# Kernel optimization log

Hardware: AMD Instinct MI355X
Metric: run time of the kernel (lower is better)

Reference implementation:

```python
import jax, jax.numpy as jnp
import numpy as np

N_NODES = 100000
N_EDGES = 1600000
C = 256            # in_channels == out_channels
NUM_BUNDLES = 64
BUNDLE_DIM = 2
NUM_GRAPHS = 128
BN_EPS = 1e-5


def setup_inputs() -> dict:
    key = jax.random.key(0)
    ks = jax.random.split(key, 12)
    x = jax.random.normal(ks[0], (N_NODES, C), dtype=jnp.float32)
    edge_index = jax.random.randint(ks[1], (2, N_EDGES), 0, N_NODES, dtype=jnp.int64)
    batch = jnp.sort(jax.random.randint(ks[2], (N_NODES,), 0, NUM_GRAPHS, dtype=jnp.int64))
    s = 0.05
    # struct_enc MLP: Linear(C, 2*NB) -> GELU -> Linear(2*NB, NB)
    se_w1 = jax.random.normal(ks[3], (C, 2 * NUM_BUNDLES), dtype=jnp.float32) * s
    se_b1 = jnp.zeros((2 * NUM_BUNDLES,), dtype=jnp.float32)
    se_w2 = jax.random.normal(ks[4], (2 * NUM_BUNDLES, NUM_BUNDLES), dtype=jnp.float32) * s
    se_b2 = jnp.zeros((NUM_BUNDLES,), dtype=jnp.float32)
    # LimConv.lin: Linear(C, C)
    lin_w = jax.random.normal(ks[5], (C, C), dtype=jnp.float32) * s
    lin_b = jnp.zeros((C,), dtype=jnp.float32)
    # BatchNorm1d affine params
    bn_gamma = jnp.ones((C,), dtype=jnp.float32)
    bn_beta = jnp.zeros((C,), dtype=jnp.float32)
    return {"x": x, "edge_index": edge_index, "batch": batch,
            "se_w1": se_w1, "se_b1": se_b1, "se_w2": se_w2, "se_b2": se_b2,
            "lin_w": lin_w, "lin_b": lin_b, "bn_gamma": bn_gamma, "bn_beta": bn_beta}


def _lim_layer(x, batch, se_w1, se_b1, se_w2, se_b2, lin_w, lin_b, bn_gamma, bn_beta):
    n = x.shape[0]
    # vector field: [N, NB, 2, fiber]
    vf = x.reshape(n, NUM_BUNDLES, BUNDLE_DIM, -1)
    # struct_enc MLP -> per-bundle angle (tanh-squashed), euler map to SO(2)
    h1 = jax.nn.gelu(x @ se_w1 + se_b1, approximate=False)
    ang = jnp.tanh(h1 @ se_w2 + se_b2)          # [N, NB]
    c, s = jnp.cos(ang), jnp.sin(ang)
    # R[n,b] = [[c,-s],[s,c]]  -> [N, NB, 2, 2]
    rot = jnp.stack([jnp.stack([c, -s], axis=-1),
                     jnp.stack([s, c], axis=-1)], axis=-2)
    # rotate fibers
    vf = jnp.einsum('nbij,nbjf->nbif', rot, vf)
    h = vf.reshape(n, C) @ lin_w + lin_b
    # global mean pool over graphs, then broadcast back to nodes
    sums = jax.ops.segment_sum(h, batch, num_segments=NUM_GRAPHS)
    cnts = jax.ops.segment_sum(jnp.ones((n,), h.dtype), batch, num_segments=NUM_GRAPHS)
    hmean = sums / jnp.maximum(cnts, 1.0)[:, None]
    h = hmean[batch]
    # inverse rotation (R^T)
    vf = h.reshape(n, NUM_BUNDLES, BUNDLE_DIM, -1)
    vf = jnp.einsum('nbji,nbjf->nbif', rot, vf)
    h = vf.reshape(n, C)
    # residual (dim_in == dim_out)
    h = x + h
    # dropout p=0 / eval -> identity. BatchNorm1d with batch statistics.
    mu = jnp.mean(h, axis=0)
    var = jnp.var(h, axis=0)
    h = (h - mu) * jax.lax.rsqrt(var + BN_EPS) * bn_gamma + bn_beta
    return h


def reference(x, edge_index, batch, se_w1, se_b1, se_w2, se_b2, lin_w, lin_b, bn_gamma, bn_beta):
    # edge_index is unused when num_gnn == 0 (struct_enc is an MLP), as in the source.
    del edge_index
    return _lim_layer(x, batch, se_w1, se_b1, se_w2, se_b2, lin_w, lin_b, bn_gamma, bn_beta)
```

## Files before the change

kernel.cpp:

```cpp
#include <hip/hip_runtime.h>
#include <hip/hip_bf16.h>
#include <math.h>

#define N_NODES 100000
#define C 256
#define NB 64
#define H1D 128
#define NG 128
#define BN_EPS 1e-5f

#define BLKN 32
#define NBLK1 (N_NODES / BLKN)

#define GREC 769

#define OFF_GSUMS 0
#define OFF_BNSUM (NG * GREC)
#define OFF_BNSQ  (OFF_BNSUM + 256)
#define ZERO_FLOATS (OFF_BNSQ + 256)
#define OFF_HMEAN ZERO_FLOATS
#define OFF_WT1   (OFF_HMEAN + NG * C)
#define OFF_WT2   (OFF_WT1 + 16896)
#define OFF_CSN   (OFF_WT2 + 4352)

#define WT1_LD 264
#define WT2_LD 136
#define XS_LD  272

typedef __attribute__((ext_vector_type(8))) short bf16x8;
typedef __attribute__((ext_vector_type(4))) float f32x4;

struct __align__(8) bf4 { __hip_bfloat16 x, y, z, w; };

__device__ __forceinline__ float bf2f(__hip_bfloat16 h) { return __bfloat162float(h); }

__device__ __forceinline__ float fast_tanh(float y) {
    float e = __expf(2.f * y);
    return 1.f - 2.f / (e + 1.f);
}
__device__ __forceinline__ float fast_gelu(float v) {
    float u = 0.7978845608f * (v + 0.044715f * v * v * v);
    return 0.5f * v * (1.f + fast_tanh(u));
}

__global__ __launch_bounds__(256)
void k0_prep(const float* __restrict__ W1, const float* __restrict__ W2,
             __hip_bfloat16* __restrict__ Wt1, __hip_bfloat16* __restrict__ Wt2)
{
    const int t0 = threadIdx.x + blockIdx.x * 256;
    const int stride = gridDim.x * 256;
    for (int i = t0; i < 128 * 256; i += stride) {
        int n = i >> 8, k = i & 255;
        Wt1[n * WT1_LD + k] = __float2bfloat16(W1[k * 128 + n]);
    }
    for (int i = t0; i < 64 * 128; i += stride) {
        int n = i >> 7, k = i & 127;
        Wt2[n * WT2_LD + k] = __float2bfloat16(W2[k * 64 + n]);
    }
}

__global__ __launch_bounds__(256, 6)
void k1_angles_rot_pool(const float* __restrict__ x,
                        const int* __restrict__ batch,
                        const __hip_bfloat16* __restrict__ Wt1g,
                        const float* __restrict__ b1,
                        const __hip_bfloat16* __restrict__ Wt2g,
                        const float* __restrict__ b2,
                        float* __restrict__ gsums,
                        float* __restrict__ bnsum, float* __restrict__ bnsq,
                        __hip_bfloat16* __restrict__ csng)
{
    __shared__ __hip_bfloat16 xs[BLKN][XS_LD];
    __shared__ char sm_u[BLKN * WT2_LD * 2];
    __shared__ int gsh[BLKN];
    auto h1s = (__hip_bfloat16 (*)[WT2_LD])sm_u;
    auto csn = (__hip_bfloat16 (*)[132])sm_u;

    const int t = threadIdx.x;
    const int w = t >> 6;
    const int l = t & 63;
    const int lo = l & 15, quad = l >> 4;
    const int n0 = blockIdx.x * BLKN;

    #pragma unroll
    for (int m = 0; m < 8; ++m) {
        int idx = t + m * 256;
        int r = idx >> 6, c4 = (idx & 63) * 4;
        float4 v = *(const float4*)(x + (size_t)(n0 + r) * C + c4);
        bf4 pk;
        pk.x = __float2bfloat16(v.x); pk.y = __float2bfloat16(v.y);
        pk.z = __float2bfloat16(v.z); pk.w = __float2bfloat16(v.w);
        *(bf4*)&xs[r][c4] = pk;
    }
    if (t < BLKN) gsh[t] = batch[n0 + t];
    __syncthreads();

    const short* w1base = (const short*)Wt1g + (w * 32 + lo) * WT1_LD + quad * 8;
    f32x4 acc1[2][2];
    #pragma unroll
    for (int mt = 0; mt < 2; ++mt) { acc1[mt][0] = (f32x4)0.f; acc1[mt][1] = (f32x4)0.f; }
    #pragma unroll
    for (int k = 0; k < 8; ++k) {
        bf16x8 bA = *(const bf16x8*)(w1base + k * 32);
        bf16x8 bB = *(const bf16x8*)(w1base + 16 * WT1_LD + k * 32);
        #pragma unroll
        for (int mt = 0; mt < 2; ++mt) {
            bf16x8 afr = *(const bf16x8*)&xs[mt * 16 + lo][k * 32 + quad * 8];
            acc1[mt][0] = __builtin_amdgcn_mfma_f32_16x16x32_bf16(afr, bA, acc1[mt][0], 0, 0, 0);
            acc1[mt][1] = __builtin_amdgcn_mfma_f32_16x16x32_bf16(afr, bB, acc1[mt][1], 0, 0, 0);
        }
    }
    #pragma unroll
    for (int nt = 0; nt < 2; ++nt) {
        const float bb = b1[w * 32 + nt * 16 + lo];
        #pragma unroll
        for (int mt = 0; mt < 2; ++mt) {
            #pragma unroll
            for (int r = 0; r < 4; ++r) {
                float v = fast_gelu(acc1[mt][nt][r] + bb);
                h1s[mt * 16 + quad * 4 + r][w * 32 + nt * 16 + lo] = __float2bfloat16(v);
            }
        }
    }
    __syncthreads();

    const int mw = w >> 1;
    const int nb0 = (w & 1) * 32;
    const short* w2base = (const short*)Wt2g + (nb0 + lo) * WT2_LD + quad * 8;
    f32x4 acc2[2];
    acc2[0] = (f32x4)0.f; acc2[1] = (f32x4)0.f;
    #pragma unroll
    for (int k = 0; k < 4; ++k) {
        bf16x8 afr = *(const bf16x8*)&h1s[mw * 16 + lo][k * 32 + quad * 8];
        bf16x8 bA = *(const bf16x8*)(w2base + k * 32);
        bf16x8 bB = *(const bf16x8*)(w2base + 16 * WT2_LD + k * 32);
        acc2[0] = __builtin_amdgcn_mfma_f32_16x16x32_bf16(afr, bA, acc2[0], 0, 0, 0);
        acc2[1] = __builtin_amdgcn_mfma_f32_16x16x32_bf16(afr, bB, acc2[1], 0, 0, 0);
    }
    __syncthreads();

    #pragma unroll
    for (int nt = 0; nt < 2; ++nt) {
        const int col = nb0 + nt * 16 + lo;
        const float bb = b2[col];
        #pragma unroll
        for (int r = 0; r < 4; ++r) {
            float a = fast_tanh(acc2[nt][r] + bb);
            union { unsigned int u; __hip_bfloat16 h[2]; } p;
            p.h[0] = __float2bfloat16(__cosf(a));
            p.h[1] = __float2bfloat16(__sinf(a));
            *(unsigned int*)&csn[mw * 16 + quad * 4 + r][2 * col] = p.u;
        }
    }
    __syncthreads();

    #pragma unroll
    for (int m = 0; m < 4; ++m) {
        int idx = t + m * 256;
        int row = idx >> 5;
        int q = (idx & 31);
        uint2 v = *(const uint2*)&csn[row][q * 4];
        *(uint2*)(csng + (size_t)(n0 + row) * 128 + q * 4) = v;
    }

    {
        const int c = t;
        const int b = c >> 2;
        const int idx2 = c & 3;
        float xc_a = 0.f, xs_a = 0.f, xm = 0.f, xq = 0.f, st = 0.f, rcnt = 0.f;
        int gprev = gsh[0];
        #pragma unroll 8
        for (int r = 0; r < BLKN; ++r) {
            const int g = gsh[r];
            if (g != gprev) {
                float* rec = gsums + (size_t)gprev * GREC;
                atomicAdd(&rec[c], xc_a);
                atomicAdd(&rec[256 + c], xs_a);
                atomicAdd(&rec[512 + t], st);
                if (t == 0) atomicAdd(&rec[768], rcnt);
                xc_a = 0.f; xs_a = 0.f; st = 0.f; rcnt = 0.f; gprev = g;
            }
            const float xv = bf2f(xs[r][c]);
            union { unsigned int u; __hip_bfloat16 h[2]; } cs;
            cs.u = *(const unsigned int*)&csn[r][2 * b];
            const float cv = bf2f(cs.h[0]);
            const float sv = bf2f(cs.h[1]);
            xc_a += xv * cv;
            xs_a += xv * sv;
            xm += xv;
            xq += xv * xv;
            st += (idx2 == 0) ? cv : (idx2 == 1) ? sv : (idx2 == 2) ? cv * cv : cv * sv;
            rcnt += 1.f;
        }
        float* rec = gsums + (size_t)gprev * GREC;
        atomicAdd(&rec[c], xc_a);
        atomicAdd(&rec[256 + c], xs_a);
        atomicAdd(&rec[512 + t], st);
        if (t == 0) atomicAdd(&rec[768], rcnt);
        atomicAdd(&bnsum[c], xm);
        atomicAdd(&bnsq[c], xq);
    }
}

__global__ __launch_bounds__(256)
void k2_hmean_stats(const float* __restrict__ gsums,
                    const float* __restrict__ lin_w, const float* __restrict__ lin_b,
                    float* __restrict__ hmean,
                    float* __restrict__ bnsum, float* __restrict__ bnsq)
{
    __shared__ float xc[C], xsv[C], bs4[C], grot[C], hm[C];
    __shared__ float cnt_sh;
    const int g = blockIdx.x;
    const int t = threadIdx.x;
    const float* rec = gsums + (size_t)g * GREC;
    xc[t]  = rec[t];
    xsv[t] = rec[256 + t];
    bs4[t] = rec[512 + t];
    if (t == 0) cnt_sh = rec[768];
    __syncthreads();

    const int b = t >> 2, idx2 = t & 3, i2 = idx2 >> 1;
    grot[t] = (i2 == 0) ? (xc[t] - xsv[t + 2]) : (xsv[t - 2] + xc[t]);
    __syncthreads();

    float a0 = 0.f, a1 = 0.f, a2 = 0.f, a3 = 0.f;
    #pragma unroll 4
    for (int k = 0; k < C; k += 4) {
        a0 += grot[k + 0] * lin_w[(size_t)(k + 0) * C + t];
        a1 += grot[k + 1] * lin_w[(size_t)(k + 1) * C + t];
        a2 += grot[k + 2] * lin_w[(size_t)(k + 2) * C + t];
        a3 += grot[k + 3] * lin_w[(size_t)(k + 3) * C + t];
    }
    const float cnt = cnt_sh;
    const float hv = (cnt > 0.f) ? ((a0 + a1 + a2 + a3) / cnt + lin_b[t]) : 0.f;
    hm[t] = hv;
    hmean[g * C + t] = hv;
    __syncthreads();

    if (cnt > 0.f) {
        const int f = idx2 & 1;
        const float h0 = hm[4 * b + f];
        const float h1 = hm[4 * b + 2 + f];
        const float CV = bs4[4 * b + 0], SV = bs4[4 * b + 1];
        const float CC = bs4[4 * b + 2], CS = bs4[4 * b + 3];
        const float SS = cnt - CC;
        float sumc, sqc;
        if (i2 == 0) {
            sumc = h0 * CV + h1 * SV;
            sqc  = 2.f * (h0 * xc[t] + h1 * xsv[t])
                 + h0 * h0 * CC + 2.f * h0 * h1 * CS + h1 * h1 * SS;
        } else {
            sumc = -h0 * SV + h1 * CV;
            sqc  = 2.f * (-h0 * xsv[t] + h1 * xc[t])
                 + h0 * h0 * SS - 2.f * h0 * h1 * CS + h1 * h1 * CC;
        }
        atomicAdd(&bnsum[t], sumc);
        atomicAdd(&bnsq[t], sqc);
    }
}

__global__ __launch_bounds__(256, 4)
void k4_fused(const float* __restrict__ x,
              const int* __restrict__ batch,
              const __hip_bfloat16* __restrict__ csng,
              const float* __restrict__ hmean,
              const float* __restrict__ bnsum, const float* __restrict__ bnsq,
              const float* __restrict__ gamma, const float* __restrict__ beta,
              float* __restrict__ out)
{
    __shared__ float mul_s[C], add_s[C];
    const int t = threadIdx.x;
    {
        const float inv_n = 1.0f / (float)N_NODES;
        const float mu = bnsum[t] * inv_n;
        const float var = bnsq[t] * inv_n - mu * mu;
        const float inv = rsqrtf(var + BN_EPS);
        const float m = gamma[t] * inv;
        mul_s[t] = m;
        add_s[t] = beta[t] - mu * m;
    }
    __syncthreads();
    const int s = t >> 6;
    const int cg = t & 63;
    const float4 mm = *(const float4*)&mul_s[cg * 4];
    const float4 aa = *(const float4*)&add_s[cg * 4];

    for (int base = blockIdx.x * 4; base < N_NODES; base += gridDim.x * 4) {
        const int n = base + s;
        if (n < N_NODES) {
            const int g = batch[n];
            const float4 hm = *(const float4*)(hmean + (size_t)g * C + cg * 4);
            union { unsigned int u; __hip_bfloat16 h[2]; } cs;
            cs.u = *(const unsigned int*)(csng + (size_t)n * 128 + cg * 2);
            const float cv = bf2f(cs.h[0]);
            const float sv = bf2f(cs.h[1]);
            const float4 xv = *(const float4*)(x + (size_t)n * C + cg * 4);
            float4 o;
            o.x = (xv.x + cv * hm.x + sv * hm.z) * mm.x + aa.x;
            o.y = (xv.y + cv * hm.y + sv * hm.w) * mm.y + aa.y;
            o.z = (xv.z - sv * hm.x + cv * hm.z) * mm.z + aa.z;
            o.w = (xv.w - sv * hm.y + cv * hm.w) * mm.w + aa.w;
            *(float4*)(out + (size_t)n * C + cg * 4) = o;
        }
    }
}

extern "C" void kernel_launch(void* const* d_in, const int* in_sizes, int n_in,
                              void* d_out, int out_size, void* d_ws, size_t ws_size,
                              hipStream_t stream)
{
    const float* x      = (const float*)d_in[0];
    const int* batch    = (const int*)d_in[2];
    const float* W1     = (const float*)d_in[3];
    const float* b1     = (const float*)d_in[4];
    const float* W2     = (const float*)d_in[5];
    const float* b2     = (const float*)d_in[6];
    const float* lin_w  = (const float*)d_in[7];
    const float* lin_b  = (const float*)d_in[8];
    const float* gamma  = (const float*)d_in[9];
    const float* beta   = (const float*)d_in[10];

    float* ws    = (float*)d_ws;
    float* gsums = ws + OFF_GSUMS;
    float* bnsum = ws + OFF_BNSUM;
    float* bnsq  = ws + OFF_BNSQ;
    float* hmean = ws + OFF_HMEAN;
    __hip_bfloat16* Wt1  = (__hip_bfloat16*)(ws + OFF_WT1);
    __hip_bfloat16* Wt2  = (__hip_bfloat16*)(ws + OFF_WT2);
    __hip_bfloat16* csng = (__hip_bfloat16*)(ws + OFF_CSN);
    float* out   = (float*)d_out;

    hipMemsetAsync(gsums, 0, ZERO_FLOATS * sizeof(float), stream);

    k0_prep<<<32, 256, 0, stream>>>(W1, W2, Wt1, Wt2);
    k1_angles_rot_pool<<<NBLK1, 256, 0, stream>>>(x, batch, Wt1, b1, Wt2, b2,
                                                  gsums, bnsum, bnsq, csng);
    k2_hmean_stats<<<NG, 256, 0, stream>>>(gsums, lin_w, lin_b, hmean, bnsum, bnsq);
    k4_fused<<<2048, 256, 0, stream>>>(x, batch, csng, hmean, bnsum, bnsq,
                                       gamma, beta, out);
}
```

Baseline: 320.0 us.

## Process 128 rows per block and replace BN atomics with per-block partials

Each k1 block now loops over four 32-row subtiles and keeps its group and BatchNorm accumulators across them, so it issues far fewer global atomics. The per-channel BN sum and sum-of-squares are written as per-block partials into a new workspace region, and k2 reduces them with a wave shuffle before a single atomic per channel. This targets atomic contention on the 512 BN counters and repeated group flushes. In exchange k1 launches a quarter as many blocks, each with a serial loop, and k2 does extra reduction work.

```diff
diff --git a/kernel.cpp b/kernel.cpp
--- a/kernel.cpp
+++ b/kernel.cpp
@@ -10,7 +10,10 @@
 #define BN_EPS 1e-5f
 
 #define BLKN 32
-#define NBLK1 (N_NODES / BLKN)
+#define ROWS 128
+#define SUBT 4
+#define NBLK1 ((N_NODES + ROWS - 1) / ROWS)
+#define NPART NBLK1
 
 #define GREC 769
 
@@ -22,6 +25,7 @@
 #define OFF_WT1   (OFF_HMEAN + NG * C)
 #define OFF_WT2   (OFF_WT1 + 16896)
 #define OFF_CSN   (OFF_WT2 + 4352)
+#define OFF_PBN   (OFF_CSN + N_NODES * 64)
 
 #define WT1_LD 264
 #define WT2_LD 136
@@ -67,7 +71,7 @@
                         const __hip_bfloat16* __restrict__ Wt2g,
                         const float* __restrict__ b2,
                         float* __restrict__ gsums,
-                        float* __restrict__ bnsum, float* __restrict__ bnsq,
+                        float* __restrict__ pbn,
                         __hip_bfloat16* __restrict__ csng)
 {
     __shared__ __hip_bfloat16 xs[BLKN][XS_LD];
@@ -80,105 +84,119 @@
     const int w = t >> 6;
     const int l = t & 63;
     const int lo = l & 15, quad = l >> 4;
-    const int n0 = blockIdx.x * BLKN;
-
-    #pragma unroll
-    for (int m = 0; m < 8; ++m) {
-        int idx = t + m * 256;
-        int r = idx >> 6, c4 = (idx & 63) * 4;
-        float4 v = *(const float4*)(x + (size_t)(n0 + r) * C + c4);
-        bf4 pk;
-        pk.x = __float2bfloat16(v.x); pk.y = __float2bfloat16(v.y);
-        pk.z = __float2bfloat16(v.z); pk.w = __float2bfloat16(v.w);
-        *(bf4*)&xs[r][c4] = pk;
-    }
-    if (t < BLKN) gsh[t] = batch[n0 + t];
-    __syncthreads();
 
     const short* w1base = (const short*)Wt1g + (w * 32 + lo) * WT1_LD + quad * 8;
-    f32x4 acc1[2][2];
-    #pragma unroll
-    for (int mt = 0; mt < 2; ++mt) { acc1[mt][0] = (f32x4)0.f; acc1[mt][1] = (f32x4)0.f; }
-    #pragma unroll
-    for (int k = 0; k < 8; ++k) {
-        bf16x8 bA = *(const bf16x8*)(w1base + k * 32);
-        bf16x8 bB = *(const bf16x8*)(w1base + 16 * WT1_LD + k * 32);
-        #pragma unroll
-        for (int mt = 0; mt < 2; ++mt) {
-            bf16x8 afr = *(const bf16x8*)&xs[mt * 16 + lo][k * 32 + quad * 8];
-            acc1[mt][0] = __builtin_amdgcn_mfma_f32_16x16x32_bf16(afr, bA, acc1[mt][0], 0, 0, 0);
-            acc1[mt][1] = __builtin_amdgcn_mfma_f32_16x16x32_bf16(afr, bB, acc1[mt][1], 0, 0, 0);
-        }
-    }
-    #pragma unroll
-    for (int nt = 0; nt < 2; ++nt) {
-        const float bb = b1[w * 32 + nt * 16 + lo];
-        #pragma unroll
-        for (int mt = 0; mt < 2; ++mt) {
-            #pragma unroll
-            for (int r = 0; r < 4; ++r) {
-                float v = fast_gelu(acc1[mt][nt][r] + bb);
-                h1s[mt * 16 + quad * 4 + r][w * 32 + nt * 16 + lo] = __float2bfloat16(v);
-            }
-        }
-    }
-    __syncthreads();
-
     const int mw = w >> 1;
     const int nb0 = (w & 1) * 32;
     const short* w2base = (const short*)Wt2g + (nb0 + lo) * WT2_LD + quad * 8;
-    f32x4 acc2[2];
-    acc2[0] = (f32x4)0.f; acc2[1] = (f32x4)0.f;
-    #pragma unroll
-    for (int k = 0; k < 4; ++k) {
-        bf16x8 afr = *(const bf16x8*)&h1s[mw * 16 + lo][k * 32 + quad * 8];
-        bf16x8 bA = *(const bf16x8*)(w2base + k * 32);
-        bf16x8 bB = *(const bf16x8*)(w2base + 16 * WT2_LD + k * 32);
-        acc2[0] = __builtin_amdgcn_mfma_f32_16x16x32_bf16(afr, bA, acc2[0], 0, 0, 0);
-        acc2[1] = __builtin_amdgcn_mfma_f32_16x16x32_bf16(afr, bB, acc2[1], 0, 0, 0);
-    }
-    __syncthreads();
-
-    #pragma unroll
-    for (int nt = 0; nt < 2; ++nt) {
-        const int col = nb0 + nt * 16 + lo;
-        const float bb = b2[col];
-        #pragma unroll
-        for (int r = 0; r < 4; ++r) {
-            float a = fast_tanh(acc2[nt][r] + bb);
-            union { unsigned int u; __hip_bfloat16 h[2]; } p;
-            p.h[0] = __float2bfloat16(__cosf(a));
-            p.h[1] = __float2bfloat16(__sinf(a));
-            *(unsigned int*)&csn[mw * 16 + quad * 4 + r][2 * col] = p.u;
-        }
-    }
-    __syncthreads();
-
-    #pragma unroll
-    for (int m = 0; m < 4; ++m) {
-        int idx = t + m * 256;
-        int row = idx >> 5;
-        int q = (idx & 31);
-        uint2 v = *(const uint2*)&csn[row][q * 4];
-        *(uint2*)(csng + (size_t)(n0 + row) * 128 + q * 4) = v;
-    }
-
-    {
-        const int c = t;
-        const int b = c >> 2;
-        const int idx2 = c & 3;
-        float xc_a = 0.f, xs_a = 0.f, xm = 0.f, xq = 0.f, st = 0.f, rcnt = 0.f;
-        int gprev = gsh[0];
+    const float bb1_0 = b1[w * 32 + lo];
+    const float bb1_1 = b1[w * 32 + 16 + lo];
+    const float bb2_0 = b2[nb0 + lo];
+    const float bb2_1 = b2[nb0 + 16 + lo];
+
+    const int c = t;
+    const int b = c >> 2;
+    const int idx2 = c & 3;
+    float xc_a = 0.f, xs_a = 0.f, st = 0.f, rcnt = 0.f;
+    float xm = 0.f, xq = 0.f;
+    int gprev = -1;
+
+#define FLUSH_G(gidx) do {                               \
+        float* rec = gsums + (size_t)(gidx) * GREC;      \
+        atomicAdd(&rec[c], xc_a);                        \
+        atomicAdd(&rec[256 + c], xs_a);                  \
+        atomicAdd(&rec[512 + c], st);                    \
+        if (c == 0) atomicAdd(&rec[768], rcnt);          \
+    } while (0)
+
+    for (int sub = 0; sub < SUBT; ++sub) {
+        const int n0 = blockIdx.x * ROWS + sub * BLKN;
+        if (n0 >= N_NODES) break;
+
+        #pragma unroll
+        for (int m = 0; m < 8; ++m) {
+            int idx = t + m * 256;
+            int r = idx >> 6, c4 = (idx & 63) * 4;
+            float4 v = *(const float4*)(x + (size_t)(n0 + r) * C + c4);
+            bf4 pk;
+            pk.x = __float2bfloat16(v.x); pk.y = __float2bfloat16(v.y);
+            pk.z = __float2bfloat16(v.z); pk.w = __float2bfloat16(v.w);
+            *(bf4*)&xs[r][c4] = pk;
+        }
+        if (t < BLKN) gsh[t] = batch[n0 + t];
+        __syncthreads();
+
+        f32x4 acc1[2][2];
+        #pragma unroll
+        for (int mt = 0; mt < 2; ++mt) { acc1[mt][0] = (f32x4)0.f; acc1[mt][1] = (f32x4)0.f; }
+        #pragma unroll
+        for (int k = 0; k < 8; ++k) {
+            bf16x8 bA = *(const bf16x8*)(w1base + k * 32);
+            bf16x8 bB = *(const bf16x8*)(w1base + 16 * WT1_LD + k * 32);
+            #pragma unroll
+            for (int mt = 0; mt < 2; ++mt) {
+                bf16x8 afr = *(const bf16x8*)&xs[mt * 16 + lo][k * 32 + quad * 8];
+                acc1[mt][0] = __builtin_amdgcn_mfma_f32_16x16x32_bf16(afr, bA, acc1[mt][0], 0, 0, 0);
+                acc1[mt][1] = __builtin_amdgcn_mfma_f32_16x16x32_bf16(afr, bB, acc1[mt][1], 0, 0, 0);
+            }
+        }
+        #pragma unroll
+        for (int nt = 0; nt < 2; ++nt) {
+            const float bb = nt ? bb1_1 : bb1_0;
+            #pragma unroll
+            for (int mt = 0; mt < 2; ++mt) {
+                #pragma unroll
+                for (int r = 0; r < 4; ++r) {
+                    float v = fast_gelu(acc1[mt][nt][r] + bb);
+                    h1s[mt * 16 + quad * 4 + r][w * 32 + nt * 16 + lo] = __float2bfloat16(v);
+                }
+            }
+        }
+        __syncthreads();
+
+        f32x4 acc2[2];
+        acc2[0] = (f32x4)0.f; acc2[1] = (f32x4)0.f;
+        #pragma unroll
+        for (int k = 0; k < 4; ++k) {
+            bf16x8 afr = *(const bf16x8*)&h1s[mw * 16 + lo][k * 32 + quad * 8];
+            bf16x8 bA = *(const bf16x8*)(w2base + k * 32);
+            bf16x8 bB = *(const bf16x8*)(w2base + 16 * WT2_LD + k * 32);
+            acc2[0] = __builtin_amdgcn_mfma_f32_16x16x32_bf16(afr, bA, acc2[0], 0, 0, 0);
+            acc2[1] = __builtin_amdgcn_mfma_f32_16x16x32_bf16(afr, bB, acc2[1], 0, 0, 0);
+        }
+        __syncthreads();
+
+        #pragma unroll
+        for (int nt = 0; nt < 2; ++nt) {
+            const int col = nb0 + nt * 16 + lo;
+            const float bb = nt ? bb2_1 : bb2_0;
+            #pragma unroll
+            for (int r = 0; r < 4; ++r) {
+                float a = fast_tanh(acc2[nt][r] + bb);
+                union { unsigned int u; __hip_bfloat16 h[2]; } p;
+                p.h[0] = __float2bfloat16(__cosf(a));
+                p.h[1] = __float2bfloat16(__sinf(a));
+                *(unsigned int*)&csn[mw * 16 + quad * 4 + r][2 * col] = p.u;
+            }
+        }
+        __syncthreads();
+
+        #pragma unroll
+        for (int m = 0; m < 4; ++m) {
+            int idx = t + m * 256;
+            int row = idx >> 5;
+            int q = (idx & 31);
+            uint2 v = *(const uint2*)&csn[row][q * 4];
+            *(uint2*)(csng + (size_t)(n0 + row) * 128 + q * 4) = v;
+        }
+
         #pragma unroll 8
         for (int r = 0; r < BLKN; ++r) {
             const int g = gsh[r];
             if (g != gprev) {
-                float* rec = gsums + (size_t)gprev * GREC;
-                atomicAdd(&rec[c], xc_a);
-                atomicAdd(&rec[256 + c], xs_a);
-                atomicAdd(&rec[512 + t], st);
-                if (t == 0) atomicAdd(&rec[768], rcnt);
-                xc_a = 0.f; xs_a = 0.f; st = 0.f; rcnt = 0.f; gprev = g;
+                if (gprev >= 0) FLUSH_G(gprev);
+                xc_a = 0.f; xs_a = 0.f; st = 0.f; rcnt = 0.f;
+                gprev = g;
             }
             const float xv = bf2f(xs[r][c]);
             union { unsigned int u; __hip_bfloat16 h[2]; } cs;
@@ -192,18 +210,18 @@
             st += (idx2 == 0) ? cv : (idx2 == 1) ? sv : (idx2 == 2) ? cv * cv : cv * sv;
             rcnt += 1.f;
         }
-        float* rec = gsums + (size_t)gprev * GREC;
-        atomicAdd(&rec[c], xc_a);
-        atomicAdd(&rec[256 + c], xs_a);
-        atomicAdd(&rec[512 + t], st);
-        if (t == 0) atomicAdd(&rec[768], rcnt);
-        atomicAdd(&bnsum[c], xm);
-        atomicAdd(&bnsq[c], xq);
-    }
+        __syncthreads();
+    }
+
+    if (gprev >= 0) FLUSH_G(gprev);
+    pbn[(size_t)blockIdx.x * 512 + t] = xm;
+    pbn[(size_t)blockIdx.x * 512 + 256 + t] = xq;
+#undef FLUSH_G
 }
 
 __global__ __launch_bounds__(256)
 void k2_hmean_stats(const float* __restrict__ gsums,
+                    const float* __restrict__ pbn,
                     const float* __restrict__ lin_w, const float* __restrict__ lin_b,
                     float* __restrict__ hmean,
                     float* __restrict__ bnsum, float* __restrict__ bnsq)
@@ -212,6 +230,21 @@
     __shared__ float cnt_sh;
     const int g = blockIdx.x;
     const int t = threadIdx.x;
+
+    {
+        const int ch = 4 * g + (t >> 6);
+        const int lane = t & 63;
+        float acc = 0.f;
+        for (int r = lane; r < NPART; r += 64)
+            acc += pbn[(size_t)r * 512 + ch];
+        #pragma unroll
+        for (int off = 32; off; off >>= 1) acc += __shfl_down(acc, off);
+        if (lane == 0) {
+            if (ch < 256) atomicAdd(&bnsum[ch], acc);
+            else          atomicAdd(&bnsq[ch - 256], acc);
+        }
+    }
+
     const float* rec = gsums + (size_t)g * GREC;
     xc[t]  = rec[t];
     xsv[t] = rec[256 + t];
@@ -328,14 +361,15 @@
     __hip_bfloat16* Wt1  = (__hip_bfloat16*)(ws + OFF_WT1);
     __hip_bfloat16* Wt2  = (__hip_bfloat16*)(ws + OFF_WT2);
     __hip_bfloat16* csng = (__hip_bfloat16*)(ws + OFF_CSN);
+    float* pbn   = ws + OFF_PBN;
     float* out   = (float*)d_out;
 
     hipMemsetAsync(gsums, 0, ZERO_FLOATS * sizeof(float), stream);
 
     k0_prep<<<32, 256, 0, stream>>>(W1, W2, Wt1, Wt2);
     k1_angles_rot_pool<<<NBLK1, 256, 0, stream>>>(x, batch, Wt1, b1, Wt2, b2,
-                                                  gsums, bnsum, bnsq, csng);
-    k2_hmean_stats<<<NG, 256, 0, stream>>>(gsums, lin_w, lin_b, hmean, bnsum, bnsq);
+                                                  gsums, pbn, csng);
+    k2_hmean_stats<<<NG, 256, 0, stream>>>(gsums, pbn, lin_w, lin_b, hmean, bnsum, bnsq);
     k4_fused<<<2048, 256, 0, stream>>>(x, batch, csng, hmean, bnsum, bnsq,
                                        gamma, beta, out);
 }
```

After: 320.7 us. Within noise of the previous version (+0.2%).
